# Optimization experiments

Hardware: AMD Instinct MI355X
Metric: run time of the kernel (lower is better)

## Reference

```python
import jax, jax.numpy as jnp
import numpy as np

N, E, F_IN, H, C = 10000, 320000, 256, 256, 40


def setup_inputs() -> dict:
    key = jax.random.key(0)
    ks = jax.random.split(key, 12)
    inp = {
        "x": jax.random.normal(ks[0], (N, F_IN), dtype=jnp.float32),
        "edge_index": jax.random.randint(ks[1], (2, E), 0, N, dtype=jnp.int64),
    }
    dims = [(F_IN, H), (H, H), (H, H), (H, H), (H, C)]
    for i, (din, dout) in enumerate(dims, start=1):
        scale = 1.0 / np.sqrt(din)
        inp[f"W{i}"] = jax.random.normal(ks[1 + i], (din, dout), dtype=jnp.float32) * scale
        inp[f"b{i}"] = jnp.zeros((dout,), dtype=jnp.float32)
    return inp


def _gcn_norm(edge_index, num_nodes, dtype):
    # GCNConv: add self-loops, symmetric normalization D^-1/2 (A+I) D^-1/2
    loops = jnp.arange(num_nodes, dtype=edge_index.dtype)
    src = jnp.concatenate([edge_index[0], loops])
    dst = jnp.concatenate([edge_index[1], loops])
    deg = jax.ops.segment_sum(jnp.ones_like(dst, dtype=dtype), dst, num_segments=num_nodes)
    dinv = jnp.where(deg > 0, deg ** -0.5, 0.0).astype(dtype)
    norm = dinv[src] * dinv[dst]  # [E+N]
    return src, dst, norm


def _conv(h, src, dst, norm, W, b, num_nodes):
    # linear transform then gather-scale-scatter aggregation
    h = h @ W                           # [N, dout]
    msg = h[src] * norm[:, None]        # [E+N, dout]
    return jax.ops.segment_sum(msg, dst, num_segments=num_nodes) + b


def reference(x, edge_index, W1, b1, W2, b2, W3, b3, W4, b4, W5, b5):
    num_nodes = x.shape[0]
    src, dst, norm = _gcn_norm(edge_index, num_nodes, x.dtype)
    h = jax.nn.relu(_conv(x, src, dst, norm, W1, b1, num_nodes))
    h = jax.nn.relu(_conv(h, src, dst, norm, W2, b2, num_nodes))
    h = jax.nn.relu(_conv(h, src, dst, norm, W3, b3, num_nodes))
    h = jax.nn.relu(_conv(h, src, dst, norm, W4, b4, num_nodes))
    logits = _conv(h, src, dst, norm, W5, b5, num_nodes)
    return jax.nn.log_softmax(logits, axis=1), logits
```

## Files before the change

### kernel.cpp

```cpp
#include <hip/hip_runtime.h>
#include <hip/hip_bf16.h>

#define N_NODES 10000
#define N_EDGES 320000
#define HDIM    256
#define NCLS    40

typedef __attribute__((ext_vector_type(8))) short short8;
typedef __attribute__((ext_vector_type(4))) float floatx4;
typedef unsigned long long ull;
typedef unsigned short ushort;

__device__ __forceinline__ float bf2f(ushort u) {
    union { unsigned int i; float f; } v; v.i = ((unsigned int)u) << 16; return v.f;
}
__device__ __forceinline__ ushort f2bf(float f) {
    __hip_bfloat16 h = __float2bfloat16(f);
    return *reinterpret_cast<ushort*>(&h);
}


__global__ void detect_kernel(const void* x, const void* ei, int* flags) {
    const int lane = threadIdx.x & 63;
    const ushort* u = (const ushort*)x;
    int e = (u[2 * lane] >> 7) & 0xFF;
    ull badmask = __ballot(e < 100 || e > 140);
    const int* ii = (const int*)ei;
    ull oddnz = __ballot(ii[2 * lane + 1] != 0);
    if (lane == 0) {
        flags[0] = (__popcll(badmask) >= 8) ? 1 : 0;
        flags[1] = (oddnz == 0) ? 1 : 0;
    }
}


struct PrepArgs {
    const void* x;
    const void* ei;
    const void* wsrc[10];
    ushort* wdst[10];
    int woffs[11];
    ushort* xb;
    int* src32;
    int* dst32;
    int* cnt;
    const int* flags;
};

#define PREP_XB 2500
#define PREP_WB 1069
#define PREP_EB 1250
#define PREP_ZB 40
#define PREP_TOTAL (PREP_XB + PREP_WB + PREP_EB + PREP_ZB)
#define WTOT 273448

__global__ __launch_bounds__(256)
void prep_kernel(PrepArgs a) {
    const int b = blockIdx.x;
    const int f32 = a.flags[0];
    if (b < PREP_XB) {
        int i4 = b * 256 + threadIdx.x;
        if (f32) {
            float4 v = ((const float4*)a.x)[i4];
            ull p = (ull)f2bf(v.x) | ((ull)f2bf(v.y) << 16) |
                    ((ull)f2bf(v.z) << 32) | ((ull)f2bf(v.w) << 48);
            ((ull*)a.xb)[i4] = p;
        } else {
            ((ull*)a.xb)[i4] = ((const ull*)a.x)[i4];
        }
    } else if (b < PREP_XB + PREP_WB) {
        int i = (b - PREP_XB) * 256 + threadIdx.x;
        if (i < WTOT) {
            int t = 0;
#pragma unroll
            for (int k = 1; k < 10; ++k) t += (i >= a.woffs[k]);
            int local = i - a.woffs[t];
            ushort v;
            if (f32) v = f2bf(((const float*)a.wsrc[t])[local]);
            else     v = ((const ushort*)a.wsrc[t])[local];
            a.wdst[t][local] = v;
        }
    } else if (b < PREP_XB + PREP_WB + PREP_EB) {
        int e = (b - PREP_XB - PREP_WB) * 256 + threadIdx.x;
        const int* ii = (const int*)a.ei;
        int s, d;
        if (a.flags[1]) { s = ii[2 * e]; d = ii[2 * (N_EDGES + e)]; }
        else            { s = ii[e];     d = ii[N_EDGES + e]; }
        a.src32[e] = ((unsigned)s < N_NODES) ? s : 0;
        a.dst32[e] = ((unsigned)d < N_NODES) ? d : 0;
    } else {
        int i = (b - PREP_XB - PREP_WB - PREP_EB) * 256 + threadIdx.x;
        if (i < N_NODES) a.cnt[i] = 0;
    }
}


__global__ void count_kernel(const int* __restrict__ dst, int* __restrict__ cnt) {
    int e = blockIdx.x * 256 + threadIdx.x;
    if (e < N_EDGES) atomicAdd(&cnt[dst[e]], 1);
}

__global__ __launch_bounds__(1024)
void scan_dinv_kernel(const int* __restrict__ cnt, int* __restrict__ offs,
                      int* __restrict__ woff, float* __restrict__ dinv) {
    __shared__ int part[1024];
    const int t = threadIdx.x;
    const int CH = (N_NODES + 1023) / 1024;
    const int base = t * CH;
    int s = 0;
    for (int j = 0; j < CH; ++j) {
        int i = base + j;
        if (i < N_NODES) s += cnt[i];
    }
    part[t] = s;
    __syncthreads();
    for (int off = 1; off < 1024; off <<= 1) {
        int v = 0;
        if (t >= off) v = part[t - off];
        __syncthreads();
        part[t] += v;
        __syncthreads();
    }
    int run = (t == 0) ? 0 : part[t - 1];
    for (int j = 0; j < CH; ++j) {
        int i = base + j;
        if (i < N_NODES) {
            int c = cnt[i];
            offs[i] = run;
            woff[i] = run;
            dinv[i] = rsqrtf((float)c + 1.0f);
            run += c;
        }
    }
}

__global__ void fill_kernel(const int* __restrict__ src, const int* __restrict__ dst,
                            int* __restrict__ woff, int* __restrict__ csr) {
    int e = blockIdx.x * 256 + threadIdx.x;
    if (e < N_EDGES) {
        int d = dst[e];
        int p = atomicAdd(&woff[d], 1);
        csr[p] = src[e];
    }
}


__global__ __launch_bounds__(256)
void gemm256_kernel(const ushort* __restrict__ A, const ushort* __restrict__ W,
                    const float* __restrict__ dinv, ushort* __restrict__ T) {
    const int lane = threadIdx.x & 63;
    const int wave = threadIdx.x >> 6;
    const int m = lane & 15;
    const int quad = lane >> 4;
    const int c0 = blockIdx.x * 32;

    short8 bfrag[2][8];
#pragma unroll
    for (int t = 0; t < 2; ++t)
#pragma unroll
        for (int s = 0; s < 8; ++s)
#pragma unroll
            for (int j = 0; j < 8; ++j)
                bfrag[t][s][j] = (short)W[(size_t)(s * 32 + quad * 8 + j) * 256 + c0 + t * 16 + m];

    const int step = gridDim.y * 4;
    for (int rt = blockIdx.y * 4 + wave; rt < N_NODES / 16; rt += step) {
        const int r0 = rt * 16;
        floatx4 acc0 = {0.f, 0.f, 0.f, 0.f};
        floatx4 acc1 = {0.f, 0.f, 0.f, 0.f};
        const ushort* arow = A + (size_t)(r0 + m) * 256 + quad * 8;
#pragma unroll
        for (int s = 0; s < 8; ++s) {
            short8 af = *(const short8*)(arow + s * 32);
            acc0 = __builtin_amdgcn_mfma_f32_16x16x32_bf16(af, bfrag[0][s], acc0, 0, 0, 0);
            acc1 = __builtin_amdgcn_mfma_f32_16x16x32_bf16(af, bfrag[1][s], acc1, 0, 0, 0);
        }
#pragma unroll
        for (int r = 0; r < 4; ++r) {
            int row = r0 + quad * 4 + r;
            float di = dinv[row];
            T[(size_t)row * 256 + c0 + m]      = f2bf(acc0[r] * di);
            T[(size_t)row * 256 + c0 + 16 + m] = f2bf(acc1[r] * di);
        }
    }
}


__global__ __launch_bounds__(256)
void gemm40_kernel(const ushort* __restrict__ A, const ushort* __restrict__ W,
                   const float* __restrict__ dinv, float* __restrict__ T) {
    const int lane = threadIdx.x & 63;
    const int wave = threadIdx.x >> 6;
    const int m = lane & 15;
    const int quad = lane >> 4;
    const int col = blockIdx.x * 16 + m;
    const bool colok = col < NCLS;

    short8 bfrag[8];
#pragma unroll
    for (int s = 0; s < 8; ++s)
#pragma unroll
        for (int j = 0; j < 8; ++j)
            bfrag[s][j] = colok ? (short)W[(size_t)(s * 32 + quad * 8 + j) * NCLS + col] : (short)0;

    const int step = gridDim.y * 4;
    for (int rt = blockIdx.y * 4 + wave; rt < N_NODES / 16; rt += step) {
        const int r0 = rt * 16;
        floatx4 acc = {0.f, 0.f, 0.f, 0.f};
        const ushort* arow = A + (size_t)(r0 + m) * 256 + quad * 8;
#pragma unroll
        for (int s = 0; s < 8; ++s) {
            short8 af = *(const short8*)(arow + s * 32);
            acc = __builtin_amdgcn_mfma_f32_16x16x32_bf16(af, bfrag[s], acc, 0, 0, 0);
        }
        if (colok) {
#pragma unroll
            for (int r = 0; r < 4; ++r) {
                int row = r0 + quad * 4 + r;
                T[(size_t)row * NCLS + col] = acc[r] * dinv[row];
            }
        }
    }
}


#define ACC8(r)                                  \
    a0 += bf2f((ushort)(r));                     \
    a1 += bf2f((ushort)((r) >> 16));             \
    a2 += bf2f((ushort)((r) >> 32));             \
    a3 += bf2f((ushort)((r) >> 48));

__global__ __launch_bounds__(256)
void agg256_kernel(const ushort* __restrict__ T,
                   const int* __restrict__ csr, const int* __restrict__ offs,
                   const int* __restrict__ cnt, const float* __restrict__ dinv,
                   const ushort* __restrict__ bias,
                   ushort* __restrict__ H) {
    const int node = blockIdx.x * 4 + (threadIdx.x >> 6);
    const int lane = threadIdx.x & 63;
    const int start = offs[node];
    const int count = cnt[node];
    const float di = dinv[node];

    const ushort* base = T + lane * 4;
    ull self = *(const ull*)(base + (size_t)node * 256);
    float a0 = bf2f((ushort)self);
    float a1 = bf2f((ushort)(self >> 16));
    float a2 = bf2f((ushort)(self >> 32));
    float a3 = bf2f((ushort)(self >> 48));

    for (int bj = 0; bj < count; bj += 64) {
        int mrem = count - bj;
        int mm = mrem < 64 ? mrem : 64;
        int idxv = (lane < mm) ? csr[start + bj + lane] : 0;
        int jj = 0;
        for (; jj + 4 <= mm; jj += 4) {
            int s0 = __shfl(idxv, jj + 0);
            int s1 = __shfl(idxv, jj + 1);
            int s2 = __shfl(idxv, jj + 2);
            int s3 = __shfl(idxv, jj + 3);
            ull r0 = *(const ull*)(base + (size_t)s0 * 256);
            ull r1 = *(const ull*)(base + (size_t)s1 * 256);
            ull r2 = *(const ull*)(base + (size_t)s2 * 256);
            ull r3 = *(const ull*)(base + (size_t)s3 * 256);
            ACC8(r0); ACC8(r1); ACC8(r2); ACC8(r3);
        }
        for (; jj < mm; ++jj) {
            int s = __shfl(idxv, jj);
            ull r = *(const ull*)(base + (size_t)s * 256);
            ACC8(r);
        }
    }

    ull b4 = *(const ull*)(bias + lane * 4);
    float v0 = fmaxf(a0 * di + bf2f((ushort)b4), 0.f);
    float v1 = fmaxf(a1 * di + bf2f((ushort)(b4 >> 16)), 0.f);
    float v2 = fmaxf(a2 * di + bf2f((ushort)(b4 >> 32)), 0.f);
    float v3 = fmaxf(a3 * di + bf2f((ushort)(b4 >> 48)), 0.f);
    ull pack = (ull)f2bf(v0) | ((ull)f2bf(v1) << 16) | ((ull)f2bf(v2) << 32) | ((ull)f2bf(v3) << 48);
    *(ull*)(H + (size_t)node * 256 + lane * 4) = pack;
}


__global__ __launch_bounds__(256)
void aggsoft_kernel(const float* __restrict__ T,
                    const int* __restrict__ csr, const int* __restrict__ offs,
                    const int* __restrict__ cnt, const float* __restrict__ dinv,
                    const ushort* __restrict__ bias,
                    void* __restrict__ out, const int* __restrict__ flags) {
    const int node = blockIdx.x * 4 + (threadIdx.x >> 6);
    const int lane = threadIdx.x & 63;
    const int start = offs[node];
    const int count = cnt[node];
    const float di = dinv[node];

    float acc = (lane < NCLS) ? T[(size_t)node * NCLS + lane] : 0.f;
    for (int bj = 0; bj < count; bj += 64) {
        int mrem = count - bj;
        int mm = mrem < 64 ? mrem : 64;
        int idxv = (lane < mm) ? csr[start + bj + lane] : 0;
        int jj = 0;
        for (; jj + 4 <= mm; jj += 4) {
            int s0 = __shfl(idxv, jj + 0);
            int s1 = __shfl(idxv, jj + 1);
            int s2 = __shfl(idxv, jj + 2);
            int s3 = __shfl(idxv, jj + 3);
            if (lane < NCLS) {
                float t0 = T[(size_t)s0 * NCLS + lane];
                float t1 = T[(size_t)s1 * NCLS + lane];
                float t2 = T[(size_t)s2 * NCLS + lane];
                float t3 = T[(size_t)s3 * NCLS + lane];
                acc += t0 + t1 + t2 + t3;
            }
        }
        for (; jj < mm; ++jj) {
            int s = __shfl(idxv, jj);
            if (lane < NCLS) acc += T[(size_t)s * NCLS + lane];
        }
    }

    float l = (lane < NCLS) ? (acc * di + bf2f(bias[lane])) : -INFINITY;
    float mx = l;
#pragma unroll
    for (int o = 32; o > 0; o >>= 1) mx = fmaxf(mx, __shfl_xor(mx, o));
    float e = (lane < NCLS) ? __expf(l - mx) : 0.f;
    float sum = e;
#pragma unroll
    for (int o = 32; o > 0; o >>= 1) sum += __shfl_xor(sum, o);
    float ls = l - mx - __logf(sum);
    if (lane < NCLS) {
        size_t i0 = (size_t)node * NCLS + lane;
        size_t i1 = (size_t)N_NODES * NCLS + i0;
        if (flags[0]) {
            ((float*)out)[i0] = ls;
            ((float*)out)[i1] = l;
        } else {
            ((ushort*)out)[i0] = f2bf(ls);
            ((ushort*)out)[i1] = f2bf(l);
        }
    }
}


static inline size_t alup(size_t x) { return (x + 255) & ~(size_t)255; }

extern "C" void kernel_launch(void* const* d_in, const int* in_sizes, int n_in,
                              void* d_out, int out_size, void* d_ws, size_t ws_size,
                              hipStream_t stream) {
    char* w = (char*)d_ws;
    int* flags   = (int*)w;           w += alup(16);
    float* dinv  = (float*)w;         w += alup(N_NODES * 4);
    int* cnt     = (int*)w;           w += alup(N_NODES * 4);
    int* offs    = (int*)w;           w += alup(N_NODES * 4);
    int* woff    = (int*)w;           w += alup(N_NODES * 4);
    int* src32   = (int*)w;           w += alup(N_EDGES * 4);
    int* dst32   = (int*)w;           w += alup(N_EDGES * 4);
    int* csr     = (int*)w;           w += alup(N_EDGES * 4);
    ushort* xb   = (ushort*)w;        w += alup((size_t)N_NODES * HDIM * 2);
    ushort* wb[5]; ushort* bb[5];
    for (int l = 0; l < 5; ++l) {
        int wn = (l < 4) ? HDIM * HDIM : HDIM * NCLS;
        int bn = (l < 4) ? HDIM : NCLS;
        wb[l] = (ushort*)w; w += alup((size_t)wn * 2);
        bb[l] = (ushort*)w; w += alup((size_t)bn * 2);
    }
    ushort* tbuf = (ushort*)w;        w += alup((size_t)N_NODES * HDIM * 2);
    ushort* hbuf = (ushort*)w;        w += alup((size_t)N_NODES * HDIM * 2);
    float* t5    = (float*)w;         w += alup((size_t)N_NODES * NCLS * 4);

    detect_kernel<<<1, 64, 0, stream>>>(d_in[0], d_in[1], flags);

    PrepArgs pa;
    pa.x = d_in[0];
    pa.ei = d_in[1];
    int sizes[10] = { HDIM * HDIM, HDIM, HDIM * HDIM, HDIM, HDIM * HDIM, HDIM,
                      HDIM * HDIM, HDIM, HDIM * NCLS, NCLS };
    int run = 0;
    for (int t = 0; t < 10; ++t) {
        pa.wsrc[t] = d_in[2 + t];
        pa.wdst[t] = (t & 1) ? bb[t >> 1] : wb[t >> 1];
        pa.woffs[t] = run;
        run += sizes[t];
    }
    pa.woffs[10] = run;
    pa.xb = xb; pa.src32 = src32; pa.dst32 = dst32; pa.cnt = cnt; pa.flags = flags;

    prep_kernel<<<PREP_TOTAL, 256, 0, stream>>>(pa);

    const int eblk = (N_EDGES + 255) / 256;
    count_kernel<<<eblk, 256, 0, stream>>>(dst32, cnt);
    scan_dinv_kernel<<<1, 1024, 0, stream>>>(cnt, offs, woff, dinv);
    fill_kernel<<<eblk, 256, 0, stream>>>(src32, dst32, woff, csr);

    const int aggblk = N_NODES / 4;

    gemm256_kernel<<<dim3(8, 39), 256, 0, stream>>>(xb, wb[0], dinv, tbuf);
    agg256_kernel<<<aggblk, 256, 0, stream>>>(tbuf, csr, offs, cnt, dinv, bb[0], hbuf);
    for (int l = 1; l < 4; ++l) {
        gemm256_kernel<<<dim3(8, 39), 256, 0, stream>>>(hbuf, wb[l], dinv, tbuf);
        agg256_kernel<<<aggblk, 256, 0, stream>>>(tbuf, csr, offs, cnt, dinv, bb[l], hbuf);
    }
    gemm40_kernel<<<dim3(3, 80), 256, 0, stream>>>(hbuf, wb[4], dinv, t5);
    aggsoft_kernel<<<aggblk, 256, 0, stream>>>(t5, csr, offs, cnt, dinv, bb[4], d_out, flags);
}
```

Baseline: 288.2 us.

## Split aggregation wave into half-waves using 16-byte gathers and zero pad row

The 256-wide aggregation kernel now has each half-wave gather alternate neighbour rows with 16-byte loads (8 bf16 per lane) instead of 8-byte loads per full wave. The two halves are combined with a cross-half shuffle at the end. A zeroed pad row at index N_NODES, cleared in the prep kernel, absorbs odd edge counts and the self-term slot so the inner loop needs no bounds checks. The goal is fewer, wider memory transactions and more gathers in flight. The GEMM grid's y dimension is also doubled, which assumes that kernel handles the larger grid correctly.

Result: faster. 274.2 us (-4.9%).

```diff
diff --git a/kernel.cpp b/kernel.cpp
--- a/kernel.cpp
+++ b/kernel.cpp
@@ -44,6 +44,8 @@
     int* src32;
     int* dst32;
     int* cnt;
+    ushort* tbuf;
+    ushort* hbuf;
     const int* flags;
 };
 
@@ -51,7 +53,8 @@
 #define PREP_WB 1069
 #define PREP_EB 1250
 #define PREP_ZB 40
-#define PREP_TOTAL (PREP_XB + PREP_WB + PREP_EB + PREP_ZB)
+#define PREP_SB 1
+#define PREP_TOTAL (PREP_XB + PREP_WB + PREP_EB + PREP_ZB + PREP_SB)
 #define WTOT 273448
 
 __global__ __launch_bounds__(256)
@@ -88,9 +91,13 @@
         else            { s = ii[e];     d = ii[N_EDGES + e]; }
         a.src32[e] = ((unsigned)s < N_NODES) ? s : 0;
         a.dst32[e] = ((unsigned)d < N_NODES) ? d : 0;
-    } else {
+    } else if (b < PREP_XB + PREP_WB + PREP_EB + PREP_ZB) {
         int i = (b - PREP_XB - PREP_WB - PREP_EB) * 256 + threadIdx.x;
         if (i < N_NODES) a.cnt[i] = 0;
+    } else {
+        int t = threadIdx.x;
+        if (t < 64)       ((ull*)(a.tbuf + (size_t)N_NODES * 256))[t] = 0;
+        else if (t < 128) ((ull*)(a.hbuf + (size_t)N_NODES * 256))[t - 64] = 0;
     }
 }
 
@@ -224,11 +231,17 @@
 }
 
 
-#define ACC8(r)                                  \
-    a0 += bf2f((ushort)(r));                     \
-    a1 += bf2f((ushort)((r) >> 16));             \
-    a2 += bf2f((ushort)((r) >> 32));             \
-    a3 += bf2f((ushort)((r) >> 48));
+__device__ __forceinline__ void accum16(float* acc, int4 r) {
+    int d[4] = {r.x, r.y, r.z, r.w};
+#pragma unroll
+    for (int k = 0; k < 4; ++k) {
+        union { int i; float f; } lo, hi;
+        lo.i = d[k] << 16;
+        hi.i = d[k] & 0xffff0000;
+        acc[2 * k]     += lo.f;
+        acc[2 * k + 1] += hi.f;
+    }
+}
 
 __global__ __launch_bounds__(256)
 void agg256_kernel(const ushort* __restrict__ T,
@@ -238,47 +251,65 @@
                    ushort* __restrict__ H) {
     const int node = blockIdx.x * 4 + (threadIdx.x >> 6);
     const int lane = threadIdx.x & 63;
+    const int half = lane >> 5;
+    const int q = lane & 31;
     const int start = offs[node];
     const int count = cnt[node];
     const float di = dinv[node];
 
-    const ushort* base = T + lane * 4;
-    ull self = *(const ull*)(base + (size_t)node * 256);
-    float a0 = bf2f((ushort)self);
-    float a1 = bf2f((ushort)(self >> 16));
-    float a2 = bf2f((ushort)(self >> 32));
-    float a3 = bf2f((ushort)(self >> 48));
+    float acc[8];
+    {
+        int sinit = half ? N_NODES : node;
+        int4 r = *(const int4*)(T + (size_t)sinit * 256 + q * 8);
+#pragma unroll
+        for (int k = 0; k < 4; ++k) {
+            union { int i; float f; } lo, hi;
+            int d = (&r.x)[k];
+            lo.i = d << 16; hi.i = d & 0xffff0000;
+            acc[2 * k] = lo.f; acc[2 * k + 1] = hi.f;
+        }
+    }
 
     for (int bj = 0; bj < count; bj += 64) {
         int mrem = count - bj;
         int mm = mrem < 64 ? mrem : 64;
-        int idxv = (lane < mm) ? csr[start + bj + lane] : 0;
-        int jj = 0;
-        for (; jj + 4 <= mm; jj += 4) {
-            int s0 = __shfl(idxv, jj + 0);
-            int s1 = __shfl(idxv, jj + 1);
-            int s2 = __shfl(idxv, jj + 2);
-            int s3 = __shfl(idxv, jj + 3);
-            ull r0 = *(const ull*)(base + (size_t)s0 * 256);
-            ull r1 = *(const ull*)(base + (size_t)s1 * 256);
-            ull r2 = *(const ull*)(base + (size_t)s2 * 256);
-            ull r3 = *(const ull*)(base + (size_t)s3 * 256);
-            ACC8(r0); ACC8(r1); ACC8(r2); ACC8(r3);
-        }
-        for (; jj < mm; ++jj) {
-            int s = __shfl(idxv, jj);
-            ull r = *(const ull*)(base + (size_t)s * 256);
-            ACC8(r);
-        }
-    }
-
-    ull b4 = *(const ull*)(bias + lane * 4);
-    float v0 = fmaxf(a0 * di + bf2f((ushort)b4), 0.f);
-    float v1 = fmaxf(a1 * di + bf2f((ushort)(b4 >> 16)), 0.f);
-    float v2 = fmaxf(a2 * di + bf2f((ushort)(b4 >> 32)), 0.f);
-    float v3 = fmaxf(a3 * di + bf2f((ushort)(b4 >> 48)), 0.f);
-    ull pack = (ull)f2bf(v0) | ((ull)f2bf(v1) << 16) | ((ull)f2bf(v2) << 32) | ((ull)f2bf(v3) << 48);
-    *(ull*)(H + (size_t)node * 256 + lane * 4) = pack;
+        int idxv = (lane < mm) ? csr[start + bj + lane] : N_NODES;
+        int j2 = 0;
+        for (; j2 + 8 <= mm; j2 += 8) {
+            int s0 = __shfl(idxv, j2 + half);
+            int s1 = __shfl(idxv, j2 + 2 + half);
+            int s2 = __shfl(idxv, j2 + 4 + half);
+            int s3 = __shfl(idxv, j2 + 6 + half);
+            int4 r0 = *(const int4*)(T + (size_t)s0 * 256 + q * 8);
+            int4 r1 = *(const int4*)(T + (size_t)s1 * 256 + q * 8);
+            int4 r2 = *(const int4*)(T + (size_t)s2 * 256 + q * 8);
+            int4 r3 = *(const int4*)(T + (size_t)s3 * 256 + q * 8);
+            accum16(acc, r0); accum16(acc, r1); accum16(acc, r2); accum16(acc, r3);
+        }
+        for (; j2 < mm; j2 += 2) {
+            int s = __shfl(idxv, j2 + half);
+            int4 r = *(const int4*)(T + (size_t)s * 256 + q * 8);
+            accum16(acc, r);
+        }
+    }
+
+#pragma unroll
+    for (int i = 0; i < 8; ++i) acc[i] += __shfl_xor(acc[i], 32);
+
+    if (half == 0) {
+        int4 bv = *(const int4*)(bias + q * 8);
+        int out_d[4];
+#pragma unroll
+        for (int k = 0; k < 4; ++k) {
+            union { int i; float f; } lo, hi;
+            int d = (&bv.x)[k];
+            lo.i = d << 16; hi.i = d & 0xffff0000;
+            float v0 = fmaxf(acc[2 * k] * di + lo.f, 0.f);
+            float v1 = fmaxf(acc[2 * k + 1] * di + hi.f, 0.f);
+            out_d[k] = (int)f2bf(v0) | ((int)f2bf(v1) << 16);
+        }
+        *(int4*)(H + (size_t)node * 256 + q * 8) = *(int4*)out_d;
+    }
 }
 
 
@@ -364,8 +395,8 @@
         wb[l] = (ushort*)w; w += alup((size_t)wn * 2);
         bb[l] = (ushort*)w; w += alup((size_t)bn * 2);
     }
-    ushort* tbuf = (ushort*)w;        w += alup((size_t)N_NODES * HDIM * 2);
-    ushort* hbuf = (ushort*)w;        w += alup((size_t)N_NODES * HDIM * 2);
+    ushort* tbuf = (ushort*)w;        w += alup((size_t)(N_NODES + 16) * HDIM * 2);
+    ushort* hbuf = (ushort*)w;        w += alup((size_t)(N_NODES + 16) * HDIM * 2);
     float* t5    = (float*)w;         w += alup((size_t)N_NODES * NCLS * 4);
 
     detect_kernel<<<1, 64, 0, stream>>>(d_in[0], d_in[1], flags);
@@ -383,7 +414,8 @@
         run += sizes[t];
     }
     pa.woffs[10] = run;
-    pa.xb = xb; pa.src32 = src32; pa.dst32 = dst32; pa.cnt = cnt; pa.flags = flags;
+    pa.xb = xb; pa.src32 = src32; pa.dst32 = dst32; pa.cnt = cnt;
+    pa.tbuf = tbuf; pa.hbuf = hbuf; pa.flags = flags;
 
     prep_kernel<<<PREP_TOTAL, 256, 0, stream>>>(pa);
 
@@ -394,10 +426,10 @@
 
     const int aggblk = N_NODES / 4;
 
-    gemm256_kernel<<<dim3(8, 39), 256, 0, stream>>>(xb, wb[0], dinv, tbuf);
+    gemm256_kernel<<<dim3(8, 78), 256, 0, stream>>>(xb, wb[0], dinv, tbuf);
     agg256_kernel<<<aggblk, 256, 0, stream>>>(tbuf, csr, offs, cnt, dinv, bb[0], hbuf);
     for (int l = 1; l < 4; ++l) {
-        gemm256_kernel<<<dim3(8, 39), 256, 0, stream>>>(hbuf, wb[l], dinv, tbuf);
+        gemm256_kernel<<<dim3(8, 78), 256, 0, stream>>>(hbuf, wb[l], dinv, tbuf);
         agg256_kernel<<<aggblk, 256, 0, stream>>>(tbuf, csr, offs, cnt, dinv, bb[l], hbuf);
     }
     gemm40_kernel<<<dim3(3, 80), 256, 0, stream>>>(hbuf, wb[4], dinv, t5);
```
